# Performance work log

Hardware: AMD Instinct MI355X
Metric: run time of the kernel (lower is better)

## Reference

```python
import jax, jax.numpy as jnp
import numpy as np

B, S, D, H = 2, 2048, 1024, 16
DH = D // H  # 64


def setup_inputs() -> dict:
    key = jax.random.key(0)
    ks = jax.random.split(key, 7)
    scale = 0.02
    return {
        "q": jax.random.normal(ks[0], (B, S, D), dtype=jnp.float32),
        "k": jax.random.normal(ks[1], (B, S, D), dtype=jnp.float32),
        "v": jax.random.normal(ks[2], (B, S, D), dtype=jnp.float32),
        "Wq": jax.random.normal(ks[3], (D, D), dtype=jnp.float32) * scale,
        "Wk": jax.random.normal(ks[4], (D, D), dtype=jnp.float32) * scale,
        "Wv": jax.random.normal(ks[5], (D, D), dtype=jnp.float32) * scale,
        "Wo": jax.random.normal(ks[6], (D, D), dtype=jnp.float32) * scale,
    }


def _split_heads(x):
    # [B, S, D] -> [B, H, S, DH]
    b, s, d = x.shape
    return x.reshape(b, s, H, DH).transpose(0, 2, 1, 3)


def reference(q, k, v, Wq, Wk, Wv, Wo):
    # Linear projections (torch Linear: x @ W.T, bias=False)
    qh = _split_heads(q @ Wq.T)  # [B, H, S, DH]
    kh = _split_heads(k @ Wk.T)
    vh = _split_heads(v @ Wv.T)
    # Scaled dot-product attention (manual, materializes scores as original)
    scores = jnp.einsum("bhqd,bhkd->bhqk", qh, kh) / jnp.sqrt(
        jnp.asarray(DH, dtype=qh.dtype)
    )  # [B, H, S, S]
    attn = jax.nn.softmax(scores, axis=-1)
    out = jnp.einsum("bhqk,bhkd->bhqd", attn, vh)  # [B, H, S, DH]
    # Concat heads: [B, H, S, DH] -> [B, S, D]
    out = out.transpose(0, 2, 1, 3).reshape(q.shape[0], q.shape[1], D)
    return out @ Wo.T
```

## Files before the change

### kernel.cpp

```cpp
#include <hip/hip_runtime.h>
#include <hip/hip_bf16.h>
#include <math.h>

namespace {
constexpr int Hn  = 16;
constexpr int DH  = 64;
constexpr int S   = 2048;
constexpr int D   = 1024;
constexpr int B   = 2;
constexpr int N   = B * S;
}

typedef __attribute__((ext_vector_type(8))) short bf16x8;
typedef __attribute__((ext_vector_type(4))) float f32x4;

#if defined(__has_builtin)
#if __has_builtin(__builtin_amdgcn_exp2f)
#define HAVE_EXP2_BUILTIN 1
#endif
#endif

static __device__ __forceinline__ float exp2_fast(float x) {
#ifdef HAVE_EXP2_BUILTIN
    return __builtin_amdgcn_exp2f(x);
#else
    float r;
    asm("v_exp_f32 %0, %1" : "=v"(r) : "v"(x));
    return r;
#endif
}

static __device__ __forceinline__ ushort bf16rd(float x) {
    unsigned u = __builtin_bit_cast(unsigned, x);
    return (ushort)((u + 0x8000u) >> 16);
}
static __device__ __forceinline__ float bfu2f(ushort h) {
    unsigned u = (unsigned)h << 16;
    return __builtin_bit_cast(float, u);
}
static __device__ __forceinline__ void split1(float a, ushort& h, ushort& l) {
    h = bf16rd(a);
    l = bf16rd(a - bfu2f(h));
}
static __device__ __forceinline__ unsigned pk2bf(float lo, float hi) {
    unsigned a = (__builtin_bit_cast(unsigned, lo) + 0x8000u) >> 16;
    unsigned b = (__builtin_bit_cast(unsigned, hi) + 0x8000u) & 0xFFFF0000u;
    return a | b;
}
static __device__ __forceinline__ uint4 pkrow(float4 x, float4 y) {
    uint4 r;
    r.x = pk2bf(x.x, x.y); r.y = pk2bf(x.z, x.w);
    r.z = pk2bf(y.x, y.y); r.w = pk2bf(y.z, y.w);
    return r;
}

__global__ __launch_bounds__(256) void split_w(
    const float4* __restrict__ wq, const float4* __restrict__ wk,
    const float4* __restrict__ wv, const float4* __restrict__ wo,
    ushort4* __restrict__ wqh, ushort4* __restrict__ wkh, ushort4* __restrict__ wvh,
    ushort4* __restrict__ woh, ushort4* __restrict__ wol, int n4w) {
    const int total = 4 * n4w;
    const int stride = gridDim.x * 256;
    for (int i = blockIdx.x * 256 + threadIdx.x; i < total; i += stride) {
        const int which = i / n4w;
        const int j = i - which * n4w;
        const float4* s = which == 0 ? wq : which == 1 ? wk : which == 2 ? wv : wo;
        const float4 val = s[j];
        if (which == 3) {
            ushort4 hh, ll;
            split1(val.x, hh.x, ll.x);
            split1(val.y, hh.y, ll.y);
            split1(val.z, hh.z, ll.z);
            split1(val.w, hh.w, ll.w);
            woh[j] = hh;
            wol[j] = ll;
        } else {
            ushort4* ph = which == 0 ? wqh : which == 1 ? wkh : wvh;
            ph[j] = make_ushort4(bf16rd(val.x), bf16rd(val.y), bf16rd(val.z), bf16rd(val.w));
        }
    }
}

__global__ __launch_bounds__(256) void gemm_qkv(
    const float* __restrict__ qf, const float* __restrict__ kf,
    const float* __restrict__ vf,
    const ushort* __restrict__ Wqh, const ushort* __restrict__ Wkh,
    const ushort* __restrict__ Wvh,
    ushort* __restrict__ Qbh, ushort* __restrict__ Kbh,
    ushort* __restrict__ Vtb, float qscale) {
    constexpr int BK = 32;
    constexpr int LDT = 40;
    constexpr int K = D;
    __shared__ __align__(16) ushort sA[2][128 * LDT];
    __shared__ __align__(16) ushort sB[2][128 * LDT];

    const int tid = threadIdx.x;
    const int which = blockIdx.y >> 3;
    const int m0 = blockIdx.x * 128;
    const int n0 = (blockIdx.y & 7) * 128;

    const float*  A  = which == 0 ? qf : which == 1 ? kf : vf;
    const ushort* Wh = which == 0 ? Wqh : which == 1 ? Wkh : Wvh;

    const int l   = tid & 63;
    const int wid = tid >> 6;
    const int wm  = wid >> 1;
    const int wn  = wid & 1;
    const int lm  = l & 15;
    const int g   = l >> 4;
    const int lk  = g * 8;

    const int arow0 = tid >> 2;
    const int aslot = (tid & 3) * 8;
    const float*  gA0 = A + (size_t)(m0 + arow0) * K + aslot;
    const float*  gA1 = gA0 + (size_t)64 * K;
    const ushort* gB0 = Wh + (size_t)(n0 + arow0) * K + aslot;
    const ushort* gB1 = gB0 + (size_t)64 * K;

    const f32x4 fzero = {0.f, 0.f, 0.f, 0.f};
    f32x4 acc[4][4];
#pragma unroll
    for (int mi = 0; mi < 4; ++mi)
#pragma unroll
        for (int ni = 0; ni < 4; ++ni) acc[mi][ni] = fzero;

    float4 a00 = *(const float4*)gA0, a01 = *(const float4*)(gA0 + 4);
    float4 a10 = *(const float4*)gA1, a11 = *(const float4*)(gA1 + 4);
    uint4  b0  = *(const uint4*)gB0,  b1  = *(const uint4*)gB1;

    *(uint4*)&sA[0][arow0 * LDT + aslot]        = pkrow(a00, a01);
    *(uint4*)&sA[0][(arow0 + 64) * LDT + aslot] = pkrow(a10, a11);
    *(uint4*)&sB[0][arow0 * LDT + aslot]        = b0;
    *(uint4*)&sB[0][(arow0 + 64) * LDT + aslot] = b1;
    a00 = *(const float4*)(gA0 + BK); a01 = *(const float4*)(gA0 + BK + 4);
    a10 = *(const float4*)(gA1 + BK); a11 = *(const float4*)(gA1 + BK + 4);
    b0  = *(const uint4*)(gB0 + BK);  b1  = *(const uint4*)(gB1 + BK);
    __syncthreads();

    constexpr int NS = K / BK;
    int cur = 0;
    for (int s = 0; s < NS; ++s) {
        bf16x8 ah[4], bh[4];
#pragma unroll
        for (int mi = 0; mi < 4; ++mi)
            ah[mi] = *(const bf16x8*)&sA[cur][(wm * 64 + mi * 16 + lm) * LDT + lk];
#pragma unroll
        for (int ni = 0; ni < 4; ++ni)
            bh[ni] = *(const bf16x8*)&sB[cur][(wn * 64 + ni * 16 + lm) * LDT + lk];
        __builtin_amdgcn_s_setprio(1);
#pragma unroll
        for (int mi = 0; mi < 4; ++mi)
#pragma unroll
            for (int ni = 0; ni < 4; ++ni)
                acc[mi][ni] = __builtin_amdgcn_mfma_f32_16x16x32_bf16(
                    ah[mi], bh[ni], acc[mi][ni], 0, 0, 0);
        __builtin_amdgcn_s_setprio(0);

        if (s < NS - 1) {
            const int nx = cur ^ 1;
            *(uint4*)&sA[nx][arow0 * LDT + aslot]        = pkrow(a00, a01);
            *(uint4*)&sA[nx][(arow0 + 64) * LDT + aslot] = pkrow(a10, a11);
            *(uint4*)&sB[nx][arow0 * LDT + aslot]        = b0;
            *(uint4*)&sB[nx][(arow0 + 64) * LDT + aslot] = b1;
            if (s < NS - 2) {
                const int kn = (s + 2) * BK;
                a00 = *(const float4*)(gA0 + kn); a01 = *(const float4*)(gA0 + kn + 4);
                a10 = *(const float4*)(gA1 + kn); a11 = *(const float4*)(gA1 + kn + 4);
                b0  = *(const uint4*)(gB0 + kn);  b1  = *(const uint4*)(gB1 + kn);
            }
            __syncthreads();
            cur = nx;
        }
    }

#pragma unroll
    for (int mi = 0; mi < 4; ++mi)
#pragma unroll
        for (int ni = 0; ni < 4; ++ni) {
            const int col = n0 + wn * 64 + ni * 16 + lm;
            const int rbase = m0 + wm * 64 + mi * 16 + g * 4;
            const int hh = col >> 6, dh = col & (DH - 1);
            if (which == 0) {
#pragma unroll
                for (int r = 0; r < 4; ++r) {
                    const int row = rbase + r;
                    const int bb = row >> 11, ss = row & (S - 1);
                    const size_t idx = (((size_t)(bb * Hn + hh)) * S + ss) * DH + dh;
                    Qbh[idx] = bf16rd(acc[mi][ni][r] * qscale);
                }
            } else if (which == 1) {
#pragma unroll
                for (int r = 0; r < 4; ++r) {
                    const int row = rbase + r;
                    const int bb = row >> 11, ss = row & (S - 1);
                    const size_t idx = (((size_t)(bb * Hn + hh)) * S + ss) * DH + dh;
                    Kbh[idx] = bf16rd(acc[mi][ni][r]);
                }
            } else {
                const int bb = rbase >> 11, ss = rbase & (S - 1);
                ushort4 pk;
                pk.x = bf16rd(acc[mi][ni][0]);
                pk.y = bf16rd(acc[mi][ni][1]);
                pk.z = bf16rd(acc[mi][ni][2]);
                pk.w = bf16rd(acc[mi][ni][3]);
                const size_t idx = (((size_t)(bb * Hn + hh)) * DH + dh) * S + ss;
                *(ushort4*)&Vtb[idx] = pk;
            }
        }
}

__global__ __launch_bounds__(256) void gemm_out(const ushort* __restrict__ Ah,
                                                const ushort* __restrict__ Al,
                                                const ushort* __restrict__ Wh,
                                                const ushort* __restrict__ Wl,
                                                float* __restrict__ C) {
    constexpr int BK = 32;
    constexpr int LDT = 40;
    constexpr int K = D, O = D;
    __shared__ __align__(16) ushort sAh[2][128 * LDT];
    __shared__ __align__(16) ushort sAl[2][128 * LDT];
    __shared__ __align__(16) ushort sBh[2][64 * LDT];
    __shared__ __align__(16) ushort sBl[2][64 * LDT];

    const int tid = threadIdx.x;
    const int m0 = blockIdx.x * 128;
    const int n0 = blockIdx.y * 64;

    const int l   = tid & 63;
    const int wid = tid >> 6;
    const int wm  = wid >> 1;
    const int wn  = wid & 1;
    const int lm  = l & 15;
    const int g   = l >> 4;
    const int lk  = g * 8;

    const int arow0 = tid >> 2;
    const int aslot = (tid & 3) * 8;
    const ushort* gAh0 = Ah + (size_t)(m0 + arow0) * K + aslot;
    const ushort* gAh1 = gAh0 + (size_t)64 * K;
    const ushort* gAl0 = Al + (size_t)(m0 + arow0) * K + aslot;
    const ushort* gAl1 = gAl0 + (size_t)64 * K;
    const ushort* gBh  = Wh + (size_t)(n0 + arow0) * K + aslot;
    const ushort* gBl  = Wl + (size_t)(n0 + arow0) * K + aslot;

    const f32x4 fzero = {0.f, 0.f, 0.f, 0.f};
    f32x4 acc[4][2];
#pragma unroll
    for (int mi = 0; mi < 4; ++mi)
#pragma unroll
        for (int ni = 0; ni < 2; ++ni) acc[mi][ni] = fzero;

    uint4 rA0 = *(const uint4*)gAh0, rA1 = *(const uint4*)gAh1;
    uint4 rA2 = *(const uint4*)gAl0, rA3 = *(const uint4*)gAl1;
    uint4 rB0 = *(const uint4*)gBh,  rB1 = *(const uint4*)gBl;

    *(uint4*)&sAh[0][arow0 * LDT + aslot]        = rA0;
    *(uint4*)&sAh[0][(arow0 + 64) * LDT + aslot] = rA1;
    *(uint4*)&sAl[0][arow0 * LDT + aslot]        = rA2;
    *(uint4*)&sAl[0][(arow0 + 64) * LDT + aslot] = rA3;
    *(uint4*)&sBh[0][arow0 * LDT + aslot]        = rB0;
    *(uint4*)&sBl[0][arow0 * LDT + aslot]        = rB1;
    rA0 = *(const uint4*)(gAh0 + BK); rA1 = *(const uint4*)(gAh1 + BK);
    rA2 = *(const uint4*)(gAl0 + BK); rA3 = *(const uint4*)(gAl1 + BK);
    rB0 = *(const uint4*)(gBh + BK);  rB1 = *(const uint4*)(gBl + BK);
    __syncthreads();

    constexpr int NS = K / BK;
    int cur = 0;
    for (int s = 0; s < NS; ++s) {
        bf16x8 ah[4], al[4], bh[2], bl[2];
#pragma unroll
        for (int mi = 0; mi < 4; ++mi) {
            const int row = wm * 64 + mi * 16 + lm;
            ah[mi] = *(const bf16x8*)&sAh[cur][row * LDT + lk];
            al[mi] = *(const bf16x8*)&sAl[cur][row * LDT + lk];
        }
#pragma unroll
        for (int ni = 0; ni < 2; ++ni) {
            const int rowb = wn * 32 + ni * 16 + lm;
            bh[ni] = *(const bf16x8*)&sBh[cur][rowb * LDT + lk];
            bl[ni] = *(const bf16x8*)&sBl[cur][rowb * LDT + lk];
        }
        __builtin_amdgcn_s_setprio(1);
#pragma unroll
        for (int mi = 0; mi < 4; ++mi)
#pragma unroll
            for (int ni = 0; ni < 2; ++ni) {
                acc[mi][ni] = __builtin_amdgcn_mfma_f32_16x16x32_bf16(
                    al[mi], bh[ni], acc[mi][ni], 0, 0, 0);
                acc[mi][ni] = __builtin_amdgcn_mfma_f32_16x16x32_bf16(
                    ah[mi], bl[ni], acc[mi][ni], 0, 0, 0);
                acc[mi][ni] = __builtin_amdgcn_mfma_f32_16x16x32_bf16(
                    ah[mi], bh[ni], acc[mi][ni], 0, 0, 0);
            }
        __builtin_amdgcn_s_setprio(0);

        if (s < NS - 1) {
            const int nx = cur ^ 1;
            *(uint4*)&sAh[nx][arow0 * LDT + aslot]        = rA0;
            *(uint4*)&sAh[nx][(arow0 + 64) * LDT + aslot] = rA1;
            *(uint4*)&sAl[nx][arow0 * LDT + aslot]        = rA2;
            *(uint4*)&sAl[nx][(arow0 + 64) * LDT + aslot] = rA3;
            *(uint4*)&sBh[nx][arow0 * LDT + aslot]        = rB0;
            *(uint4*)&sBl[nx][arow0 * LDT + aslot]        = rB1;
            if (s < NS - 2) {
                const int kn = (s + 2) * BK;
                rA0 = *(const uint4*)(gAh0 + kn); rA1 = *(const uint4*)(gAh1 + kn);
                rA2 = *(const uint4*)(gAl0 + kn); rA3 = *(const uint4*)(gAl1 + kn);
                rB0 = *(const uint4*)(gBh + kn);  rB1 = *(const uint4*)(gBl + kn);
            }
            __syncthreads();
            cur = nx;
        }
    }

#pragma unroll
    for (int mi = 0; mi < 4; ++mi)
#pragma unroll
        for (int ni = 0; ni < 2; ++ni) {
            const int col = n0 + wn * 32 + ni * 16 + lm;
            const int rbase = m0 + wm * 64 + mi * 16 + g * 4;
#pragma unroll
            for (int r = 0; r < 4; ++r)
                C[(size_t)(rbase + r) * O + col] = acc[mi][ni][r];
        }
}

__global__ __launch_bounds__(256) void attn_mfma(const ushort* __restrict__ Qbh,
                                                 const ushort* __restrict__ Kbh,
                                                 const ushort* __restrict__ Vt,
                                                 ushort* __restrict__ AOh,
                                                 ushort* __restrict__ AOl) {
    constexpr int LDT = 72;
    __shared__ __align__(16) ushort Ksh[2][64 * LDT];
    __shared__ __align__(16) ushort Vts[2][64 * LDT];
    __shared__ __align__(16) ushort Ps[128 * LDT];

    const int tid = threadIdx.x;
    const int l = tid & 63, w = tid >> 6;
    const int g = l >> 4, l15 = l & 15;
    const int bh = blockIdx.x;
    const int q0 = blockIdx.y * 128;
    const size_t bhb = (size_t)bh * S * DH;

    bf16x8 qh_[2][2];
#pragma unroll
    for (int qb = 0; qb < 2; ++qb)
#pragma unroll
        for (int kk = 0; kk < 2; ++kk) {
            const size_t idx = bhb + (size_t)(q0 + w * 32 + qb * 16 + l15) * DH + kk * 32 + g * 8;
            qh_[qb][kk] = *(const bf16x8*)(Qbh + idx);
        }

    const int r_st = tid >> 2;
    const int c0 = (tid & 3) * 16;
    const ushort* gKh = Kbh + bhb + (size_t)r_st * DH + c0;
    const ushort* gVt = Vt + (size_t)bh * DH * S + (size_t)r_st * S + c0;

    uint4 pk0 = *(const uint4*)gKh, pk1 = *(const uint4*)(gKh + 8);
    uint4 pv0 = *(const uint4*)gVt, pv1 = *(const uint4*)(gVt + 8);

    const f32x4 fzero = {0.f, 0.f, 0.f, 0.f};
    f32x4 o_acc[2][4];
    f32x4 l_acc[2];
#pragma unroll
    for (int qb = 0; qb < 2; ++qb) {
        l_acc[qb] = fzero;
#pragma unroll
        for (int f = 0; f < 4; ++f) o_acc[qb][f] = fzero;
    }

    bf16x8 ones;
#pragma unroll
    for (int i = 0; i < 8; ++i) ones[i] = (short)0x3F80;

    *(uint4*)&Ksh[0][r_st * LDT + c0]     = pk0;
    *(uint4*)&Ksh[0][r_st * LDT + c0 + 8] = pk1;
    *(uint4*)&Vts[0][r_st * LDT + c0]     = pv0;
    *(uint4*)&Vts[0][r_st * LDT + c0 + 8] = pv1;
    pk0 = *(const uint4*)(gKh + 64 * DH); pk1 = *(const uint4*)(gKh + 64 * DH + 8);
    pv0 = *(const uint4*)(gVt + 64);      pv1 = *(const uint4*)(gVt + 64 + 8);
    __syncthreads();

    constexpr int NT = S / 64;
    int cur = 0;
    for (int kt = 0; kt < NT; ++kt) {
        f32x4 sc[2][4];
#pragma unroll
        for (int qb = 0; qb < 2; ++qb)
#pragma unroll
            for (int f = 0; f < 4; ++f) sc[qb][f] = fzero;
#pragma unroll
        for (int kk = 0; kk < 2; ++kk) {
            bf16x8 kh[4];
#pragma unroll
            for (int f = 0; f < 4; ++f)
                kh[f] = *(const bf16x8*)&Ksh[cur][(f * 16 + l15) * LDT + kk * 32 + g * 8];
            __builtin_amdgcn_s_setprio(1);
#pragma unroll
            for (int f = 0; f < 4; ++f)
#pragma unroll
                for (int qb = 0; qb < 2; ++qb)
                    sc[qb][f] = __builtin_amdgcn_mfma_f32_16x16x32_bf16(
                        qh_[qb][kk], kh[f], sc[qb][f], 0, 0, 0);
            __builtin_amdgcn_s_setprio(0);
        }

#pragma unroll
        for (int qb = 0; qb < 2; ++qb)
#pragma unroll
            for (int f = 0; f < 4; ++f) {
#pragma unroll
                for (int r = 0; r < 4; ++r) {
                    const int prow = w * 32 + qb * 16 + g * 4 + r;
                    const int chunk = (f * 2 + (l15 >> 3)) ^ ((prow >> 2) & 7);
                    Ps[prow * LDT + chunk * 8 + (l15 & 7)] =
                        bf16rd(exp2_fast(sc[qb][f][r]));
                }
            }

#pragma unroll
        for (int kk = 0; kk < 2; ++kk) {
            const int row0 = w * 32 + l15;
            const int row1 = row0 + 16;
            const int ck = kk * 4 + g;
            const bf16x8 pa0 = *(const bf16x8*)&Ps[row0 * LDT + ((ck ^ ((row0 >> 2) & 7)) * 8)];
            const bf16x8 pa1 = *(const bf16x8*)&Ps[row1 * LDT + ((ck ^ ((row1 >> 2) & 7)) * 8)];
            __builtin_amdgcn_s_setprio(1);
            l_acc[0] = __builtin_amdgcn_mfma_f32_16x16x32_bf16(pa0, ones, l_acc[0], 0, 0, 0);
            l_acc[1] = __builtin_amdgcn_mfma_f32_16x16x32_bf16(pa1, ones, l_acc[1], 0, 0, 0);
#pragma unroll
            for (int f = 0; f < 4; ++f) {
                const bf16x8 vt = *(const bf16x8*)&Vts[cur][(f * 16 + l15) * LDT + kk * 32 + g * 8];
                o_acc[0][f] = __builtin_amdgcn_mfma_f32_16x16x32_bf16(pa0, vt, o_acc[0][f], 0, 0, 0);
                o_acc[1][f] = __builtin_amdgcn_mfma_f32_16x16x32_bf16(pa1, vt, o_acc[1][f], 0, 0, 0);
            }
            __builtin_amdgcn_s_setprio(0);
        }

        if (kt < NT - 1) {
            const int nx = cur ^ 1;
            *(uint4*)&Ksh[nx][r_st * LDT + c0]     = pk0;
            *(uint4*)&Ksh[nx][r_st * LDT + c0 + 8] = pk1;
            *(uint4*)&Vts[nx][r_st * LDT + c0]     = pv0;
            *(uint4*)&Vts[nx][r_st * LDT + c0 + 8] = pv1;
            if (kt < NT - 2) {
                const int ok = (kt + 2) * 64 * DH;
                const int ov = (kt + 2) * 64;
                pk0 = *(const uint4*)(gKh + ok); pk1 = *(const uint4*)(gKh + ok + 8);
                pv0 = *(const uint4*)(gVt + ov); pv1 = *(const uint4*)(gVt + ov + 8);
            }
            __syncthreads();
            cur = nx;
        }
    }

    const int bb = bh >> 4, hh = bh & 15;
#pragma unroll
    for (int qb = 0; qb < 2; ++qb)
#pragma unroll
        for (int r = 0; r < 4; ++r) {
            const float inv = 1.f / l_acc[qb][r];
            const int row = q0 + w * 32 + qb * 16 + g * 4 + r;
#pragma unroll
            for (int f = 0; f < 4; ++f) {
                const float val = o_acc[qb][f][r] * inv;
                const size_t idx = ((size_t)(bb * S + row)) * D + hh * DH + f * 16 + l15;
                ushort hi, lo;
                split1(val, hi, lo);
                AOh[idx] = hi;
                AOl[idx] = lo;
            }
        }
}

extern "C" void kernel_launch(void* const* d_in, const int* in_sizes, int n_in,
                              void* d_out, int out_size, void* d_ws, size_t ws_size,
                              hipStream_t stream) {
    (void)in_sizes; (void)n_in; (void)out_size; (void)ws_size;
    const float* q  = (const float*)d_in[0];
    const float* k  = (const float*)d_in[1];
    const float* v  = (const float*)d_in[2];
    const float* Wq = (const float*)d_in[3];
    const float* Wk = (const float*)d_in[4];
    const float* Wv = (const float*)d_in[5];
    const float* Wo = (const float*)d_in[6];
    float* out = (float*)d_out;

    uint8_t* w8 = (uint8_t*)d_ws;
    constexpr size_t MB = 1u << 20;
    ushort* Wqh = (ushort*)(w8 + 0 * MB);
    ushort* Wkh = (ushort*)(w8 + 2 * MB);
    ushort* Wvh = (ushort*)(w8 + 4 * MB);
    ushort* Woh = (ushort*)(w8 + 6 * MB);
    ushort* Wol = (ushort*)(w8 + 8 * MB);
    ushort* Qbh = (ushort*)(w8 + 16 * MB);
    ushort* Kbh = (ushort*)(w8 + 24 * MB);
    ushort* Vtb = (ushort*)(w8 + 32 * MB);
    ushort* AOh = (ushort*)(w8 + 40 * MB);
    ushort* AOl = (ushort*)(w8 + 48 * MB);

    const int n4_w = (D * D) / 4;
    const dim3 blk(256);

    split_w<<<1024, blk, 0, stream>>>(
        (const float4*)Wq, (const float4*)Wk, (const float4*)Wv, (const float4*)Wo,
        (ushort4*)Wqh, (ushort4*)Wkh, (ushort4*)Wvh,
        (ushort4*)Woh, (ushort4*)Wol, n4_w);

    const float qscale = 0.125f * 1.4426950408889634f;
    gemm_qkv<<<dim3(N / 128, 24), blk, 0, stream>>>(
        q, k, v, Wqh, Wkh, Wvh, Qbh, Kbh, Vtb, qscale);

    attn_mfma<<<dim3(B * Hn, S / 128), blk, 0, stream>>>(
        Qbh, Kbh, Vtb, AOh, AOl);

    gemm_out<<<dim3(N / 128, D / 64), blk, 0, stream>>>(AOh, AOl, Woh, Wol, out);
}
```

Before: 146.9 us.

## Pre-convert activations to bf16 and stage tiles via direct global-to-LDS loads

Activations q/k/v are now converted to bf16 in a separate pre-pass merged with the weight split. This lets gemm_qkv load bf16 tiles straight into shared memory with global_load_lds and XOR-swizzled layouts, replacing register-staged double buffering. The attention kernel likewise stages K and V^T tiles with async global-to-LDS loads into unpadded swizzled buffers, prefetching the next tile. The trade-off is an extra full read and write pass over the activations. gemm_qkv also drops to a single LDS buffer with two barriers per k-step, so load latency is no longer overlapped there.

After: 154.6 us. 1.05x slower.

```diff
diff --git a/kernel.cpp b/kernel.cpp
--- a/kernel.cpp
+++ b/kernel.cpp
@@ -42,80 +42,84 @@
     h = bf16rd(a);
     l = bf16rd(a - bfu2f(h));
 }
-static __device__ __forceinline__ unsigned pk2bf(float lo, float hi) {
-    unsigned a = (__builtin_bit_cast(unsigned, lo) + 0x8000u) >> 16;
-    unsigned b = (__builtin_bit_cast(unsigned, hi) + 0x8000u) & 0xFFFF0000u;
-    return a | b;
-}
-static __device__ __forceinline__ uint4 pkrow(float4 x, float4 y) {
-    uint4 r;
-    r.x = pk2bf(x.x, x.y); r.y = pk2bf(x.z, x.w);
-    r.z = pk2bf(y.x, y.y); r.w = pk2bf(y.z, y.w);
-    return r;
-}
-
-__global__ __launch_bounds__(256) void split_w(
+
+static __device__ __forceinline__ void gload16(const ushort* g, ushort* l) {
+    __builtin_amdgcn_global_load_lds((const unsigned int*)g, (unsigned int*)l, 16, 0, 0);
+}
+
+__global__ __launch_bounds__(256) void split_all(
+    const float4* __restrict__ q, const float4* __restrict__ k, const float4* __restrict__ v,
     const float4* __restrict__ wq, const float4* __restrict__ wk,
     const float4* __restrict__ wv, const float4* __restrict__ wo,
+    ushort4* __restrict__ qh, ushort4* __restrict__ kh, ushort4* __restrict__ vh,
     ushort4* __restrict__ wqh, ushort4* __restrict__ wkh, ushort4* __restrict__ wvh,
-    ushort4* __restrict__ woh, ushort4* __restrict__ wol, int n4w) {
-    const int total = 4 * n4w;
+    ushort4* __restrict__ woh, ushort4* __restrict__ wol,
+    int n4a, int n4w) {
+    const int total = 3 * n4a + 4 * n4w;
     const int stride = gridDim.x * 256;
     for (int i = blockIdx.x * 256 + threadIdx.x; i < total; i += stride) {
-        const int which = i / n4w;
-        const int j = i - which * n4w;
-        const float4* s = which == 0 ? wq : which == 1 ? wk : which == 2 ? wv : wo;
-        const float4 val = s[j];
-        if (which == 3) {
-            ushort4 hh, ll;
-            split1(val.x, hh.x, ll.x);
-            split1(val.y, hh.y, ll.y);
-            split1(val.z, hh.z, ll.z);
-            split1(val.w, hh.w, ll.w);
-            woh[j] = hh;
-            wol[j] = ll;
+        if (i < 3 * n4a) {
+            const int which = i / n4a;
+            const int j = i - which * n4a;
+            const float4 val = (which == 0 ? q : which == 1 ? k : v)[j];
+            ushort4* ph = which == 0 ? qh : which == 1 ? kh : vh;
+            ph[j] = make_ushort4(bf16rd(val.x), bf16rd(val.y), bf16rd(val.z), bf16rd(val.w));
         } else {
-            ushort4* ph = which == 0 ? wqh : which == 1 ? wkh : wvh;
-            ph[j] = make_ushort4(bf16rd(val.x), bf16rd(val.y), bf16rd(val.z), bf16rd(val.w));
+            const int t = i - 3 * n4a;
+            const int which = t / n4w;
+            const int j = t - which * n4w;
+            const float4 val = (which == 0 ? wq : which == 1 ? wk : which == 2 ? wv : wo)[j];
+            if (which == 3) {
+                ushort4 hh, ll;
+                split1(val.x, hh.x, ll.x);
+                split1(val.y, hh.y, ll.y);
+                split1(val.z, hh.z, ll.z);
+                split1(val.w, hh.w, ll.w);
+                woh[j] = hh;
+                wol[j] = ll;
+            } else {
+                ushort4* ph = which == 0 ? wqh : which == 1 ? wkh : wvh;
+                ph[j] = make_ushort4(bf16rd(val.x), bf16rd(val.y), bf16rd(val.z), bf16rd(val.w));
+            }
         }
     }
 }
 
 __global__ __launch_bounds__(256) void gemm_qkv(
-    const float* __restrict__ qf, const float* __restrict__ kf,
-    const float* __restrict__ vf,
+    const ushort* __restrict__ qbf, const ushort* __restrict__ kbf,
+    const ushort* __restrict__ vbf,
     const ushort* __restrict__ Wqh, const ushort* __restrict__ Wkh,
     const ushort* __restrict__ Wvh,
     ushort* __restrict__ Qbh, ushort* __restrict__ Kbh,
     ushort* __restrict__ Vtb, float qscale) {
     constexpr int BK = 32;
-    constexpr int LDT = 40;
     constexpr int K = D;
-    __shared__ __align__(16) ushort sA[2][128 * LDT];
-    __shared__ __align__(16) ushort sB[2][128 * LDT];
+    __shared__ __align__(16) ushort sA[128 * BK];
+    __shared__ __align__(16) ushort sB[128 * BK];
 
     const int tid = threadIdx.x;
     const int which = blockIdx.y >> 3;
     const int m0 = blockIdx.x * 128;
     const int n0 = (blockIdx.y & 7) * 128;
 
-    const float*  A  = which == 0 ? qf : which == 1 ? kf : vf;
-    const ushort* Wh = which == 0 ? Wqh : which == 1 ? Wkh : Wvh;
-
-    const int l   = tid & 63;
-    const int wid = tid >> 6;
-    const int wm  = wid >> 1;
-    const int wn  = wid & 1;
-    const int lm  = l & 15;
-    const int g   = l >> 4;
-    const int lk  = g * 8;
-
-    const int arow0 = tid >> 2;
-    const int aslot = (tid & 3) * 8;
-    const float*  gA0 = A + (size_t)(m0 + arow0) * K + aslot;
-    const float*  gA1 = gA0 + (size_t)64 * K;
-    const ushort* gB0 = Wh + (size_t)(n0 + arow0) * K + aslot;
-    const ushort* gB1 = gB0 + (size_t)64 * K;
+    const ushort* A = which == 0 ? qbf : which == 1 ? kbf : vbf;
+    const ushort* W = which == 0 ? Wqh : which == 1 ? Wkh : Wvh;
+
+    const int l  = tid & 63;
+    const int w  = tid >> 6;
+    const int wm = w >> 1, wn = w & 1;
+    const int lm = l & 15, g = l >> 4;
+
+    const int srow = l >> 2;
+    const int schunk = (l & 3) ^ ((l >> 3) & 3);
+    const ushort* gA0 = A + (size_t)(m0 + w * 32 + srow) * K + schunk * 8;
+    const ushort* gA1 = gA0 + (size_t)16 * K;
+    const ushort* gB0 = W + (size_t)(n0 + w * 32 + srow) * K + schunk * 8;
+    const ushort* gB1 = gB0 + (size_t)16 * K;
+    ushort* lA0 = &sA[(w * 32) * BK];
+    ushort* lA1 = &sA[(w * 32 + 16) * BK];
+    ushort* lB0 = &sB[(w * 32) * BK];
+    ushort* lB1 = &sB[(w * 32 + 16) * BK];
 
     const f32x4 fzero = {0.f, 0.f, 0.f, 0.f};
     f32x4 acc[4][4];
@@ -124,29 +128,24 @@
 #pragma unroll
         for (int ni = 0; ni < 4; ++ni) acc[mi][ni] = fzero;
 
-    float4 a00 = *(const float4*)gA0, a01 = *(const float4*)(gA0 + 4);
-    float4 a10 = *(const float4*)gA1, a11 = *(const float4*)(gA1 + 4);
-    uint4  b0  = *(const uint4*)gB0,  b1  = *(const uint4*)gB1;
-
-    *(uint4*)&sA[0][arow0 * LDT + aslot]        = pkrow(a00, a01);
-    *(uint4*)&sA[0][(arow0 + 64) * LDT + aslot] = pkrow(a10, a11);
-    *(uint4*)&sB[0][arow0 * LDT + aslot]        = b0;
-    *(uint4*)&sB[0][(arow0 + 64) * LDT + aslot] = b1;
-    a00 = *(const float4*)(gA0 + BK); a01 = *(const float4*)(gA0 + BK + 4);
-    a10 = *(const float4*)(gA1 + BK); a11 = *(const float4*)(gA1 + BK + 4);
-    b0  = *(const uint4*)(gB0 + BK);  b1  = *(const uint4*)(gB1 + BK);
-    __syncthreads();
-
-    constexpr int NS = K / BK;
-    int cur = 0;
-    for (int s = 0; s < NS; ++s) {
+    const int sswz = (lm >> 1) & 3;
+
+    for (int s = 0; s < K / BK; ++s) {
+        const int k0 = s * BK;
+        if (s) __syncthreads();
+        gload16(gA0 + k0, lA0);
+        gload16(gA1 + k0, lA1);
+        gload16(gB0 + k0, lB0);
+        gload16(gB1 + k0, lB1);
+        __syncthreads();
+
         bf16x8 ah[4], bh[4];
 #pragma unroll
         for (int mi = 0; mi < 4; ++mi)
-            ah[mi] = *(const bf16x8*)&sA[cur][(wm * 64 + mi * 16 + lm) * LDT + lk];
+            ah[mi] = *(const bf16x8*)&sA[(wm * 64 + mi * 16 + lm) * BK + (g ^ sswz) * 8];
 #pragma unroll
         for (int ni = 0; ni < 4; ++ni)
-            bh[ni] = *(const bf16x8*)&sB[cur][(wn * 64 + ni * 16 + lm) * LDT + lk];
+            bh[ni] = *(const bf16x8*)&sB[(wn * 64 + ni * 16 + lm) * BK + (g ^ sswz) * 8];
         __builtin_amdgcn_s_setprio(1);
 #pragma unroll
         for (int mi = 0; mi < 4; ++mi)
@@ -155,22 +154,6 @@
                 acc[mi][ni] = __builtin_amdgcn_mfma_f32_16x16x32_bf16(
                     ah[mi], bh[ni], acc[mi][ni], 0, 0, 0);
         __builtin_amdgcn_s_setprio(0);
-
-        if (s < NS - 1) {
-            const int nx = cur ^ 1;
-            *(uint4*)&sA[nx][arow0 * LDT + aslot]        = pkrow(a00, a01);
-            *(uint4*)&sA[nx][(arow0 + 64) * LDT + aslot] = pkrow(a10, a11);
-            *(uint4*)&sB[nx][arow0 * LDT + aslot]        = b0;
-            *(uint4*)&sB[nx][(arow0 + 64) * LDT + aslot] = b1;
-            if (s < NS - 2) {
-                const int kn = (s + 2) * BK;
-                a00 = *(const float4*)(gA0 + kn); a01 = *(const float4*)(gA0 + kn + 4);
-                a10 = *(const float4*)(gA1 + kn); a11 = *(const float4*)(gA1 + kn + 4);
-                b0  = *(const uint4*)(gB0 + kn);  b1  = *(const uint4*)(gB1 + kn);
-            }
-            __syncthreads();
-            cur = nx;
-        }
     }
 
 #pragma unroll
@@ -331,10 +314,10 @@
                                                  const ushort* __restrict__ Vt,
                                                  ushort* __restrict__ AOh,
                                                  ushort* __restrict__ AOl) {
-    constexpr int LDT = 72;
-    __shared__ __align__(16) ushort Ksh[2][64 * LDT];
-    __shared__ __align__(16) ushort Vts[2][64 * LDT];
-    __shared__ __align__(16) ushort Ps[128 * LDT];
+    constexpr int PLDT = 72;
+    __shared__ __align__(16) ushort Ksh[2][64 * 64];
+    __shared__ __align__(16) ushort Vts[2][64 * 64];
+    __shared__ __align__(16) ushort Ps[128 * PLDT];
 
     const int tid = threadIdx.x;
     const int l = tid & 63, w = tid >> 6;
@@ -352,13 +335,13 @@
             qh_[qb][kk] = *(const bf16x8*)(Qbh + idx);
         }
 
-    const int r_st = tid >> 2;
-    const int c0 = (tid & 3) * 16;
-    const ushort* gKh = Kbh + bhb + (size_t)r_st * DH + c0;
-    const ushort* gVt = Vt + (size_t)bh * DH * S + (size_t)r_st * S + c0;
-
-    uint4 pk0 = *(const uint4*)gKh, pk1 = *(const uint4*)(gKh + 8);
-    uint4 pv0 = *(const uint4*)gVt, pv1 = *(const uint4*)(gVt + 8);
+    const int srow = l >> 3;
+    const int schunk = (l & 7) ^ ((l >> 3) & 7);
+    const ushort* Vb = Vt + (size_t)bh * DH * S;
+    const ushort* gK0 = Kbh + bhb + (size_t)(w * 16 + srow) * DH + schunk * 8;
+    const ushort* gK1 = gK0 + (size_t)8 * DH;
+    const ushort* gV0 = Vb + (size_t)(w * 16 + srow) * S + schunk * 8;
+    const ushort* gV1 = gV0 + (size_t)8 * S;
 
     const f32x4 fzero = {0.f, 0.f, 0.f, 0.f};
     f32x4 o_acc[2][4];
@@ -374,17 +357,24 @@
 #pragma unroll
     for (int i = 0; i < 8; ++i) ones[i] = (short)0x3F80;
 
-    *(uint4*)&Ksh[0][r_st * LDT + c0]     = pk0;
-    *(uint4*)&Ksh[0][r_st * LDT + c0 + 8] = pk1;
-    *(uint4*)&Vts[0][r_st * LDT + c0]     = pv0;
-    *(uint4*)&Vts[0][r_st * LDT + c0 + 8] = pv1;
-    pk0 = *(const uint4*)(gKh + 64 * DH); pk1 = *(const uint4*)(gKh + 64 * DH + 8);
-    pv0 = *(const uint4*)(gVt + 64);      pv1 = *(const uint4*)(gVt + 64 + 8);
+    auto stage = [&](int buf, int kt) {
+        const size_t ko = (size_t)kt * 64 * DH;
+        const size_t vo = (size_t)kt * 64;
+        gload16(gK0 + ko, &Ksh[buf][(w * 16) * 64]);
+        gload16(gK1 + ko, &Ksh[buf][(w * 16 + 8) * 64]);
+        gload16(gV0 + vo, &Vts[buf][(w * 16) * 64]);
+        gload16(gV1 + vo, &Vts[buf][(w * 16 + 8) * 64]);
+    };
+
+    stage(0, 0);
     __syncthreads();
 
     constexpr int NT = S / 64;
     int cur = 0;
+    const int rsw = l15 & 7;
     for (int kt = 0; kt < NT; ++kt) {
+        if (kt < NT - 1) stage(cur ^ 1, kt + 1);
+
         f32x4 sc[2][4];
 #pragma unroll
         for (int qb = 0; qb < 2; ++qb)
@@ -395,7 +385,7 @@
             bf16x8 kh[4];
 #pragma unroll
             for (int f = 0; f < 4; ++f)
-                kh[f] = *(const bf16x8*)&Ksh[cur][(f * 16 + l15) * LDT + kk * 32 + g * 8];
+                kh[f] = *(const bf16x8*)&Ksh[cur][(f * 16 + l15) * 64 + ((kk * 4 + g) ^ rsw) * 8];
             __builtin_amdgcn_s_setprio(1);
 #pragma unroll
             for (int f = 0; f < 4; ++f)
@@ -414,7 +404,7 @@
                 for (int r = 0; r < 4; ++r) {
                     const int prow = w * 32 + qb * 16 + g * 4 + r;
                     const int chunk = (f * 2 + (l15 >> 3)) ^ ((prow >> 2) & 7);
-                    Ps[prow * LDT + chunk * 8 + (l15 & 7)] =
+                    Ps[prow * PLDT + chunk * 8 + (l15 & 7)] =
                         bf16rd(exp2_fast(sc[qb][f][r]));
                 }
             }
@@ -424,14 +414,14 @@
             const int row0 = w * 32 + l15;
             const int row1 = row0 + 16;
             const int ck = kk * 4 + g;
-            const bf16x8 pa0 = *(const bf16x8*)&Ps[row0 * LDT + ((ck ^ ((row0 >> 2) & 7)) * 8)];
-            const bf16x8 pa1 = *(const bf16x8*)&Ps[row1 * LDT + ((ck ^ ((row1 >> 2) & 7)) * 8)];
+            const bf16x8 pa0 = *(const bf16x8*)&Ps[row0 * PLDT + ((ck ^ ((row0 >> 2) & 7)) * 8)];
+            const bf16x8 pa1 = *(const bf16x8*)&Ps[row1 * PLDT + ((ck ^ ((row1 >> 2) & 7)) * 8)];
             __builtin_amdgcn_s_setprio(1);
             l_acc[0] = __builtin_amdgcn_mfma_f32_16x16x32_bf16(pa0, ones, l_acc[0], 0, 0, 0);
             l_acc[1] = __builtin_amdgcn_mfma_f32_16x16x32_bf16(pa1, ones, l_acc[1], 0, 0, 0);
 #pragma unroll
             for (int f = 0; f < 4; ++f) {
-                const bf16x8 vt = *(const bf16x8*)&Vts[cur][(f * 16 + l15) * LDT + kk * 32 + g * 8];
+                const bf16x8 vt = *(const bf16x8*)&Vts[cur][(f * 16 + l15) * 64 + ((kk * 4 + g) ^ rsw) * 8];
                 o_acc[0][f] = __builtin_amdgcn_mfma_f32_16x16x32_bf16(pa0, vt, o_acc[0][f], 0, 0, 0);
                 o_acc[1][f] = __builtin_amdgcn_mfma_f32_16x16x32_bf16(pa1, vt, o_acc[1][f], 0, 0, 0);
             }
@@ -439,19 +429,8 @@
         }
 
         if (kt < NT - 1) {
-            const int nx = cur ^ 1;
-            *(uint4*)&Ksh[nx][r_st * LDT + c0]     = pk0;
-            *(uint4*)&Ksh[nx][r_st * LDT + c0 + 8] = pk1;
-            *(uint4*)&Vts[nx][r_st * LDT + c0]     = pv0;
-            *(uint4*)&Vts[nx][r_st * LDT + c0 + 8] = pv1;
-            if (kt < NT - 2) {
-                const int ok = (kt + 2) * 64 * DH;
-                const int ov = (kt + 2) * 64;
-                pk0 = *(const uint4*)(gKh + ok); pk1 = *(const uint4*)(gKh + ok + 8);
-                pv0 = *(const uint4*)(gVt + ov); pv1 = *(const uint4*)(gVt + ov + 8);
-            }
             __syncthreads();
-            cur = nx;
+            cur ^= 1;
         }
     }
 
@@ -494,23 +473,30 @@
     ushort* Wvh = (ushort*)(w8 + 4 * MB);
     ushort* Woh = (ushort*)(w8 + 6 * MB);
     ushort* Wol = (ushort*)(w8 + 8 * MB);
-    ushort* Qbh = (ushort*)(w8 + 16 * MB);
-    ushort* Kbh = (ushort*)(w8 + 24 * MB);
-    ushort* Vtb = (ushort*)(w8 + 32 * MB);
-    ushort* AOh = (ushort*)(w8 + 40 * MB);
-    ushort* AOl = (ushort*)(w8 + 48 * MB);
-
-    const int n4_w = (D * D) / 4;
+    ushort* qbf = (ushort*)(w8 + 16 * MB);
+    ushort* kbf = (ushort*)(w8 + 24 * MB);
+    ushort* vbf = (ushort*)(w8 + 32 * MB);
+    ushort* Qbh = (ushort*)(w8 + 40 * MB);
+    ushort* Kbh = (ushort*)(w8 + 48 * MB);
+    ushort* Vtb = (ushort*)(w8 + 56 * MB);
+    ushort* AOh = (ushort*)(w8 + 64 * MB);
+    ushort* AOl = (ushort*)(w8 + 72 * MB);
+
+    const int n4_act = (N * D) / 4;
+    const int n4_w   = (D * D) / 4;
     const dim3 blk(256);
 
-    split_w<<<1024, blk, 0, stream>>>(
+    split_all<<<2048, blk, 0, stream>>>(
+        (const float4*)q, (const float4*)k, (const float4*)v,
         (const float4*)Wq, (const float4*)Wk, (const float4*)Wv, (const float4*)Wo,
+        (ushort4*)qbf, (ushort4*)kbf, (ushort4*)vbf,
         (ushort4*)Wqh, (ushort4*)Wkh, (ushort4*)Wvh,
-        (ushort4*)Woh, (ushort4*)Wol, n4_w);
+        (ushort4*)Woh, (ushort4*)Wol,
+        n4_act, n4_w);
 
     const float qscale = 0.125f * 1.4426950408889634f;
     gemm_qkv<<<dim3(N / 128, 24), blk, 0, stream>>>(
-        q, k, v, Wqh, Wkh, Wvh, Qbh, Kbh, Vtb, qscale);
+        qbf, kbf, vbf, Wqh, Wkh, Wvh, Qbh, Kbh, Vtb, qscale);
 
     attn_mfma<<<dim3(B * Hn, S / 128), blk, 0, stream>>>(
         Qbh, Kbh, Vtb, AOh, AOl);
```
